# Optimization experiments

Measured on AMD Instinct MI355X. Metric: run time of the kernel, lower is better.

## Reference

```python
import jax, jax.numpy as jnp
import numpy as np

B, C, T, D = 32, 1024, 64, 64
F_OUT = 128      # out_channels
S_DIM = 64       # stage_dim
N_STG = 5        # num_stages
H_MLP = 64       # hidden of stage_mlp


def setup_inputs() -> dict:
    key = jax.random.key(0)
    ks = jax.random.split(key, 16)
    sc = 0.05
    return {
        "x": jax.random.normal(ks[0], (B, C, T, D), dtype=jnp.float32),
        "A_init": jax.random.uniform(ks[1], (C, C), dtype=jnp.float32),
        "W_proj": jax.random.normal(ks[2], (F_OUT, D), dtype=jnp.float32) * sc,
        "b_proj": jnp.zeros((F_OUT,), dtype=jnp.float32),
        "W_s1": jax.random.normal(ks[3], (H_MLP, D), dtype=jnp.float32) * sc,
        "b_s1": jnp.zeros((H_MLP,), dtype=jnp.float32),
        "W_s2": jax.random.normal(ks[4], (N_STG, H_MLP), dtype=jnp.float32) * sc,
        "b_s2": jnp.zeros((N_STG,), dtype=jnp.float32),
        "W_c1": jax.random.normal(ks[5], (S_DIM, N_STG), dtype=jnp.float32) * sc,
        "b_c1": jnp.zeros((S_DIM,), dtype=jnp.float32),
        "W_c2": jax.random.normal(ks[6], (S_DIM, S_DIM), dtype=jnp.float32) * sc,
        "b_c2": jnp.zeros((S_DIM,), dtype=jnp.float32),
        "att": jax.random.normal(ks[7], (2 * F_OUT + S_DIM,), dtype=jnp.float32) * sc,
        "lam": jnp.array([0.5], dtype=jnp.float32),
    }


def reference(x, A_init, W_proj, b_proj, W_s1, b_s1, W_s2, b_s2,
              W_c1, b_c1, W_c2, b_c2, att, lam):
    F = W_proj.shape[0]
    x_red = jnp.mean(x, axis=2)                               # (B,C,D)
    Z = x_red @ W_proj.T + b_proj                             # (B,C,F)
    x_glob = jnp.mean(x_red, axis=1)                          # (B,D)
    s = jax.nn.softmax(
        jax.nn.relu(x_glob @ W_s1.T + b_s1) @ W_s2.T + b_s2, axis=-1)  # (B,num_stages)
    c = jax.nn.relu(s @ W_c1.T + b_c1) @ W_c2.T + b_c2        # (B,stage_dim)
    # Split att_weight: sum over concat([Z_i, Z_j, c]) * att == dot-per-part
    a_i, a_j, a_c = att[:F], att[F:2 * F], att[2 * F:]
    e = ((Z @ a_i)[:, :, None]            # (B,C,1) broadcast over j
         + (Z @ a_j)[:, None, :]          # (B,1,C) broadcast over i
         + (c @ a_c)[:, None, None])      # (B,1,1)
    e = jax.nn.leaky_relu(e, negative_slope=0.2)              # (B,C,C)
    eps = 1e-8
    e_tilde = e + lam[0] * jnp.log(A_init + eps)[None, :, :]
    alpha = jax.nn.softmax(e_tilde, axis=-1)                  # (B,C,C)
    h = alpha @ Z                                             # (B,C,F)
    return h, s
```

## Files before the change

kernel.cpp:

```cpp
#include <hip/hip_runtime.h>
#include <hip/hip_fp16.h>
#include <cstddef>
#include <math.h>


typedef __attribute__((ext_vector_type(8))) short bf16x8;
typedef __attribute__((ext_vector_type(4))) float f32x4;

__device__ inline unsigned f2bf(float f) {
  unsigned u = __float_as_uint(f);
  return (u + 0x7FFFu + ((u >> 16) & 1u)) >> 16;
}

#define LOGA_OFF 0u
#define EI_OFF   524288u
#define EJ_OFF   557056u
#define PXG_OFF  589824u
#define ZK_OFF   655360u

__global__ __launch_bounds__(256) void k_fuse1(
    const float4* __restrict__ X4, const float* __restrict__ A,
    const float* __restrict__ lam, const float* __restrict__ W,
    const float* __restrict__ bproj, const float* __restrict__ att,
    uint4* __restrict__ Zk, float* __restrict__ ei, float* __restrict__ ej,
    float4* __restrict__ pXG4, __half* __restrict__ llogA) {
  int tid = threadIdx.x;
  int bk = blockIdx.x;
  if (bk >= 1024) {
    float l = lam[0];
    int row = bk - 1024;
    const float4* Arow = (const float4*)(A + (size_t)row * 1024);
    float4 a = Arow[tid];
    __half2 h0 = __floats2half2_rn(l * __logf(a.x + 1e-8f),
                                   l * __logf(a.y + 1e-8f));
    __half2 h1 = __floats2half2_rn(l * __logf(a.z + 1e-8f),
                                   l * __logf(a.w + 1e-8f));
    union { __half2 h[2]; uint2 u; } pk;
    pk.h[0] = h0; pk.h[1] = h1;
    ((uint2*)llogA)[(size_t)row * 256 + tid] = pk.u;
    return;
  }
  __shared__ float Wl[64 * 129];
  __shared__ float4 xr4[32 * 16];
  int rb = bk * 32;

#pragma unroll
  for (int k = 0; k < 32; ++k) {
    int g = k * 256 + tid;
    Wl[(g & 63) * 129 + (g >> 6)] = W[g];
  }

  {
    int row = tid >> 3, g = tid & 7;
    const float4* xbase = X4 + ((size_t)(rb + row)) * 1024 + g;
    float4 a0 = make_float4(0.f, 0.f, 0.f, 0.f), a1 = a0;
#pragma unroll
    for (int k = 0; k < 128; k += 2) {
      float4 v0 = xbase[k * 8];
      float4 v1 = xbase[k * 8 + 8];
      a0.x += v0.x; a0.y += v0.y; a0.z += v0.z; a0.w += v0.w;
      a1.x += v1.x; a1.y += v1.y; a1.z += v1.z; a1.w += v1.w;
    }
    const float inv = 1.0f / 64.0f;
    a0.x *= inv; a0.y *= inv; a0.z *= inv; a0.w *= inv;
    a1.x *= inv; a1.y *= inv; a1.z *= inv; a1.w *= inv;
    xr4[row * 16 + g] = a0;
    xr4[row * 16 + g + 8] = a1;
  }
  __syncthreads();

  if (tid < 16) {
    float4 p = make_float4(0.f, 0.f, 0.f, 0.f);
#pragma unroll
    for (int r = 0; r < 32; ++r) {
      float4 v = xr4[r * 16 + tid];
      p.x += v.x; p.y += v.y; p.z += v.z; p.w += v.w;
    }
    pXG4[bk * 16 + tid] = p;
  }

  int f = tid & 127, rg = tid >> 7;
  float wreg[64];
#pragma unroll
  for (int d = 0; d < 64; ++d) wreg[d] = Wl[d * 129 + f];
  float bias = bproj[f];
  float acc[16];
#pragma unroll
  for (int r = 0; r < 16; ++r) acc[r] = bias;
#pragma unroll
  for (int r = 0; r < 16; ++r) {
    int row = rg * 16 + r;
#pragma unroll
    for (int dq = 0; dq < 16; ++dq) {
      float4 xv = xr4[row * 16 + dq];
      acc[r] = fmaf(wreg[dq * 4 + 0], xv.x, acc[r]);
      acc[r] = fmaf(wreg[dq * 4 + 1], xv.y, acc[r]);
      acc[r] = fmaf(wreg[dq * 4 + 2], xv.z, acc[r]);
      acc[r] = fmaf(wreg[dq * 4 + 3], xv.w, acc[r]);
    }
  }
  int b = rb >> 10;
  int cbase = (rb & 1023) + rg * 16;
#pragma unroll
  for (int k2 = 0; k2 < 2; ++k2) {
    unsigned w0 = f2bf(acc[k2 * 8 + 0]) | (f2bf(acc[k2 * 8 + 1]) << 16);
    unsigned w1 = f2bf(acc[k2 * 8 + 2]) | (f2bf(acc[k2 * 8 + 3]) << 16);
    unsigned w2 = f2bf(acc[k2 * 8 + 4]) | (f2bf(acc[k2 * 8 + 5]) << 16);
    unsigned w3 = f2bf(acc[k2 * 8 + 6]) | (f2bf(acc[k2 * 8 + 7]) << 16);
    size_t chunk = ((size_t)b * 128 + ((cbase >> 3) + k2)) * 128 + f;
    Zk[chunk] = make_uint4(w0, w1, w2, w3);
  }
  __syncthreads();
  float* Zl = Wl;
#pragma unroll
  for (int r = 0; r < 16; ++r)
    Zl[(rg * 16 + r) * 130 + f] = acc[r];
  __syncthreads();
  int row = tid >> 3, g = tid & 7;
  float si = 0.f, sj = 0.f;
#pragma unroll
  for (int u = 0; u < 16; ++u) {
    float z = Zl[row * 130 + g * 16 + u];
    si = fmaf(z, att[g * 16 + u], si);
    sj = fmaf(z, att[128 + g * 16 + u], sj);
  }
  si += __shfl_xor(si, 1); sj += __shfl_xor(sj, 1);
  si += __shfl_xor(si, 2); sj += __shfl_xor(sj, 2);
  si += __shfl_xor(si, 4); sj += __shfl_xor(sj, 4);
  if (g == 0) { ei[rb + row] = si; ej[rb + row] = sj; }
}

__global__ __launch_bounds__(64) void k_main(const uint4* __restrict__ Zk,
    const __half* __restrict__ llogA, const float* __restrict__ ei,
    const float* __restrict__ ej, const float* __restrict__ pXG,
    const float* __restrict__ Ws1, const float* __restrict__ bs1,
    const float* __restrict__ Ws2, const float* __restrict__ bs2,
    const float* __restrict__ Wc1, const float* __restrict__ bc1,
    const float* __restrict__ Wc2, const float* __restrict__ bc2,
    const float* __restrict__ att,
    float* __restrict__ hout, float* __restrict__ sout) {
  int bid = blockIdx.x;
  int b = ((bid & 7) << 2) | ((bid >> 3) & 3);
  int rowgrp = bid >> 5;
  int i0 = rowgrp * 16;
  int lane = threadIdx.x;
  int lg = lane >> 4, ln = lane & 15;

  float ecb;
  {
    float xg = 0.f;
    const float* pb = pXG + (size_t)b * 32 * 64;
#pragma unroll 8
    for (int p = 0; p < 32; ++p) xg += pb[p * 64 + lane];
    xg *= (1.0f / 1024.0f);
    const float* w1 = Ws1 + lane * 64;
    float h = bs1[lane];
#pragma unroll 16
    for (int d = 0; d < 64; ++d) h = fmaf(__shfl(xg, d), w1[d], h);
    h = fmaxf(h, 0.f);
    int ln5 = lane < 5 ? lane : 4;
    const float* w2 = Ws2 + ln5 * 64;
    float l = bs2[ln5];
#pragma unroll 16
    for (int k = 0; k < 64; ++k) l = fmaf(__shfl(h, k), w2[k], l);
    float s0 = __shfl(l, 0), s1 = __shfl(l, 1), s2 = __shfl(l, 2),
          s3 = __shfl(l, 3), s4 = __shfl(l, 4);
    float m = fmaxf(fmaxf(fmaxf(s0, s1), fmaxf(s2, s3)), s4);
    float e0 = __expf(s0 - m), e1 = __expf(s1 - m), e2 = __expf(s2 - m),
          e3 = __expf(s3 - m), e4 = __expf(s4 - m);
    float inv = 1.0f / (e0 + e1 + e2 + e3 + e4);
    s0 = e0 * inv; s1 = e1 * inv; s2 = e2 * inv; s3 = e3 * inv; s4 = e4 * inv;
    if (rowgrp == 0 && lane == 0) {
      sout[b * 5 + 0] = s0; sout[b * 5 + 1] = s1; sout[b * 5 + 2] = s2;
      sout[b * 5 + 3] = s3; sout[b * 5 + 4] = s4;
    }
    const float* wc1 = Wc1 + lane * 5;
    float cv = bc1[lane];
    cv = fmaf(s0, wc1[0], cv); cv = fmaf(s1, wc1[1], cv);
    cv = fmaf(s2, wc1[2], cv); cv = fmaf(s3, wc1[3], cv);
    cv = fmaf(s4, wc1[4], cv);
    cv = fmaxf(cv, 0.f);
    const float* wc2 = Wc2 + lane * 64;
    float c2 = bc2[lane];
#pragma unroll 16
    for (int k = 0; k < 64; ++k) c2 = fmaf(__shfl(cv, k), wc2[k], c2);
    float v = c2 * att[256 + lane];
#pragma unroll
    for (int o = 32; o; o >>= 1) v += __shfl_xor(v, o);
    ecb = v;
  }

  int i_gl = i0 + ln;
  float eir = ei[b * 1024 + i_gl];
  const uint4*  lrowH = (const uint4*)(llogA + (size_t)i_gl * 1024);
  const float4* ejr4  = (const float4*)(ej + b * 1024);
  const uint4*  ZkB   = Zk + (size_t)b * 128 * 128;

  float m_run = -1e30f, s_run = 0.0f;
  f32x4 acc[8];
#pragma unroll
  for (int q = 0; q < 8; ++q) { f32x4 z = {0.f, 0.f, 0.f, 0.f}; acc[q] = z; }

  for (int jt = 0; jt < 16; ++jt) {
    int j0 = jt * 64;
    uint4 bz[2][8];
#pragma unroll
    for (int ks = 0; ks < 2; ++ks)
#pragma unroll
      for (int fb = 0; fb < 8; ++fb)
        bz[ks][fb] = ZkB[(size_t)((j0 >> 3) + ks * 4 + lg) * 128 + fb * 16 + ln];
    float tv[16];
    float tm = -1e30f;
#pragma unroll
    for (int ks = 0; ks < 2; ++ks) {
      int jb = (j0 + ks * 32 + lg * 8) >> 2;
      float4 e0 = ejr4[jb], e1 = ejr4[jb + 1];
      union { uint4 u; __half2 h[4]; } lu;
      lu.u = lrowH[jb >> 1];
      float2 f0 = __half22float2(lu.h[0]);
      float2 f1 = __half22float2(lu.h[1]);
      float2 f2 = __half22float2(lu.h[2]);
      float2 f3 = __half22float2(lu.h[3]);
      float eq[8] = {e0.x, e0.y, e0.z, e0.w, e1.x, e1.y, e1.z, e1.w};
      float lq[8] = {f0.x, f0.y, f1.x, f1.y, f2.x, f2.y, f3.x, f3.y};
#pragma unroll
      for (int u = 0; u < 8; ++u) {
        float t = eir + eq[u] + ecb;
        t = t > 0.0f ? t : 0.2f * t;
        t += lq[u];
        tv[ks * 8 + u] = t;
        tm = fmaxf(tm, t);
      }
    }
    tm = fmaxf(tm, __shfl_xor(tm, 16));
    tm = fmaxf(tm, __shfl_xor(tm, 32));
    float newm = fmaxf(m_run, tm);
    float scale = __expf(m_run - newm);
    float ts = 0.0f;
    unsigned pw[8];
#pragma unroll
    for (int q = 0; q < 8; ++q) {
      float p0 = __expf(tv[2 * q] - newm);
      float p1 = __expf(tv[2 * q + 1] - newm);
      ts += p0 + p1;
      pw[q] = f2bf(p0) | (f2bf(p1) << 16);
    }
    ts += __shfl_xor(ts, 16);
    ts += __shfl_xor(ts, 32);
    s_run = s_run * scale + ts;
    m_run = newm;
#pragma unroll
    for (int q = 0; q < 8; ++q) acc[q] *= scale;
    union { unsigned u[4]; bf16x8 v; } c0, c1;
#pragma unroll
    for (int q = 0; q < 4; ++q) { c0.u[q] = pw[q]; c1.u[q] = pw[4 + q]; }
#pragma unroll
    for (int fb = 0; fb < 8; ++fb)
      acc[fb] = __builtin_amdgcn_mfma_f32_16x16x32_bf16(c0.v, *(bf16x8*)&bz[0][fb], acc[fb], 0, 0, 0);
#pragma unroll
    for (int fb = 0; fb < 8; ++fb)
      acc[fb] = __builtin_amdgcn_mfma_f32_16x16x32_bf16(c1.v, *(bf16x8*)&bz[1][fb], acc[fb], 0, 0, 0);
  }

  float invs = 1.0f / s_run;
  float inv_m[4];
#pragma unroll
  for (int r = 0; r < 4; ++r) inv_m[r] = __shfl(invs, lg * 4 + r);
  float* hb = hout + ((size_t)b * 1024 + i0 + lg * 4) * 128 + ln;
#pragma unroll
  for (int fb = 0; fb < 8; ++fb) {
#pragma unroll
    for (int r = 0; r < 4; ++r)
      hb[(size_t)r * 128 + fb * 16] = acc[fb][r] * inv_m[r];
  }
}

extern "C" void kernel_launch(void* const* d_in, const int* in_sizes, int n_in,
                              void* d_out, int out_size, void* d_ws, size_t ws_size,
                              hipStream_t stream) {
  const float* x     = (const float*)d_in[0];
  const float* Ainit = (const float*)d_in[1];
  const float* Wproj = (const float*)d_in[2];
  const float* bproj = (const float*)d_in[3];
  const float* Ws1   = (const float*)d_in[4];
  const float* bs1   = (const float*)d_in[5];
  const float* Ws2   = (const float*)d_in[6];
  const float* bs2   = (const float*)d_in[7];
  const float* Wc1   = (const float*)d_in[8];
  const float* bc1   = (const float*)d_in[9];
  const float* Wc2   = (const float*)d_in[10];
  const float* bc2   = (const float*)d_in[11];
  const float* att   = (const float*)d_in[12];
  const float* lam   = (const float*)d_in[13];

  float* ws    = (float*)d_ws;
  __half* llogA = (__half*)(ws + LOGA_OFF);
  float* ei    = ws + EI_OFF;
  float* ej    = ws + EJ_OFF;
  float* pXG   = ws + PXG_OFF;
  uint4* Zk    = (uint4*)(ws + ZK_OFF);

  float* hout = (float*)d_out;
  float* sout = hout + (size_t)32 * 1024 * 128;

  hipLaunchKernelGGL(k_fuse1, dim3(2048), dim3(256), 0, stream,
                     (const float4*)x, Ainit, lam, Wproj, bproj, att,
                     Zk, ei, ej, (float4*)pXG, llogA);
  hipLaunchKernelGGL(k_main,  dim3(2048), dim3(64),  0, stream,
                     Zk, llogA, ei, ej, pXG,
                     Ws1, bs1, Ws2, bs2, Wc1, bc1, Wc2, bc2, att,
                     hout, sout);
}
```

Measured before the change: 178.8 us.

## Fold log(A) blocks into projection blocks and coalesce x mean-over-T loads

```diff
diff --git a/kernel.cpp b/kernel.cpp
--- a/kernel.cpp
+++ b/kernel.cpp
@@ -26,24 +26,23 @@
     float4* __restrict__ pXG4, __half* __restrict__ llogA) {
   int tid = threadIdx.x;
   int bk = blockIdx.x;
-  if (bk >= 1024) {
-    float l = lam[0];
-    int row = bk - 1024;
-    const float4* Arow = (const float4*)(A + (size_t)row * 1024);
-    float4 a = Arow[tid];
-    __half2 h0 = __floats2half2_rn(l * __logf(a.x + 1e-8f),
-                                   l * __logf(a.y + 1e-8f));
-    __half2 h1 = __floats2half2_rn(l * __logf(a.z + 1e-8f),
-                                   l * __logf(a.w + 1e-8f));
-    union { __half2 h[2]; uint2 u; } pk;
-    pk.h[0] = h0; pk.h[1] = h1;
-    ((uint2*)llogA)[(size_t)row * 256 + tid] = pk.u;
-    return;
-  }
   __shared__ float Wl[64 * 129];
   __shared__ float4 xr4[32 * 16];
   int rb = bk * 32;
 
+  {
+    float lv = lam[0];
+    const float4* Arow = (const float4*)(A + (size_t)bk * 1024);
+    float4 a = Arow[tid];
+    __half2 h0 = __floats2half2_rn(lv * __logf(a.x + 1e-8f),
+                                   lv * __logf(a.y + 1e-8f));
+    __half2 h1 = __floats2half2_rn(lv * __logf(a.z + 1e-8f),
+                                   lv * __logf(a.w + 1e-8f));
+    union { __half2 h[2]; uint2 u; } pk;
+    pk.h[0] = h0; pk.h[1] = h1;
+    ((uint2*)llogA)[(size_t)bk * 256 + tid] = pk.u;
+  }
+
 #pragma unroll
   for (int k = 0; k < 32; ++k) {
     int g = k * 256 + tid;
@@ -51,21 +50,46 @@
   }
 
   {
-    int row = tid >> 3, g = tid & 7;
-    const float4* xbase = X4 + ((size_t)(rb + row)) * 1024 + g;
-    float4 a0 = make_float4(0.f, 0.f, 0.f, 0.f), a1 = a0;
-#pragma unroll
-    for (int k = 0; k < 128; k += 2) {
-      float4 v0 = xbase[k * 8];
-      float4 v1 = xbase[k * 8 + 8];
+    int w = tid >> 6, l = tid & 63;
+    int tg = l >> 4, dq = l & 15;
+    int r0 = w * 8;
+    const float4* base = X4 + ((size_t)(rb + r0)) * 1024 + l;
+    float4 a0 = make_float4(0.f, 0.f, 0.f, 0.f);
+    float4 a1 = a0, a2 = a0, a3 = a0, a4 = a0, a5 = a0, a6 = a0, a7 = a0;
+#pragma unroll
+    for (int s = 0; s < 16; ++s) {
+      int o = s * 64;
+      float4 v0 = base[0 * 1024 + o];
+      float4 v1 = base[1 * 1024 + o];
+      float4 v2 = base[2 * 1024 + o];
+      float4 v3 = base[3 * 1024 + o];
+      float4 v4 = base[4 * 1024 + o];
+      float4 v5 = base[5 * 1024 + o];
+      float4 v6 = base[6 * 1024 + o];
+      float4 v7 = base[7 * 1024 + o];
       a0.x += v0.x; a0.y += v0.y; a0.z += v0.z; a0.w += v0.w;
       a1.x += v1.x; a1.y += v1.y; a1.z += v1.z; a1.w += v1.w;
-    }
+      a2.x += v2.x; a2.y += v2.y; a2.z += v2.z; a2.w += v2.w;
+      a3.x += v3.x; a3.y += v3.y; a3.z += v3.z; a3.w += v3.w;
+      a4.x += v4.x; a4.y += v4.y; a4.z += v4.z; a4.w += v4.w;
+      a5.x += v5.x; a5.y += v5.y; a5.z += v5.z; a5.w += v5.w;
+      a6.x += v6.x; a6.y += v6.y; a6.z += v6.z; a6.w += v6.w;
+      a7.x += v7.x; a7.y += v7.y; a7.z += v7.z; a7.w += v7.w;
+    }
+    float4 ar[8] = {a0, a1, a2, a3, a4, a5, a6, a7};
     const float inv = 1.0f / 64.0f;
-    a0.x *= inv; a0.y *= inv; a0.z *= inv; a0.w *= inv;
-    a1.x *= inv; a1.y *= inv; a1.z *= inv; a1.w *= inv;
-    xr4[row * 16 + g] = a0;
-    xr4[row * 16 + g + 8] = a1;
+#pragma unroll
+    for (int r = 0; r < 8; ++r) {
+      float4 a = ar[r];
+      a.x += __shfl_xor(a.x, 16); a.y += __shfl_xor(a.y, 16);
+      a.z += __shfl_xor(a.z, 16); a.w += __shfl_xor(a.w, 16);
+      a.x += __shfl_xor(a.x, 32); a.y += __shfl_xor(a.y, 32);
+      a.z += __shfl_xor(a.z, 32); a.w += __shfl_xor(a.w, 32);
+      if (tg == 0) {
+        a.x *= inv; a.y *= inv; a.z *= inv; a.w *= inv;
+        xr4[(r0 + r) * 16 + dq] = a;
+      }
+    }
   }
   __syncthreads();
 
@@ -303,7 +327,7 @@
   float* hout = (float*)d_out;
   float* sout = hout + (size_t)32 * 1024 * 128;
 
-  hipLaunchKernelGGL(k_fuse1, dim3(2048), dim3(256), 0, stream,
+  hipLaunchKernelGGL(k_fuse1, dim3(1024), dim3(256), 0, stream,
                      (const float4*)x, Ainit, lam, Wproj, bproj, att,
                      Zk, ei, ej, (float4*)pXG, llogA);
   hipLaunchKernelGGL(k_main,  dim3(2048), dim3(64),  0, stream,
```

Result: no change. 182.0 us (+1.8%).
